# Kernel tuning notes

Measured on AMD Instinct MI355X. Metric: run time of the kernel, lower is better.

## Reference

```python
import jax, jax.numpy as jnp
import numpy as np

WEIGHT_BITS = 5
QUANT_BITS = 16
BN_EPS = 1e-5


def _quant_weight_pow2(w):
    # Round weights to signed powers of two; exponent clipped per DeepShift:
    # shift range = [-(2^(bits-1)-2), 0] = [-14, 0] for 5-bit weights.
    shift_min = -(2 ** (WEIGHT_BITS - 1) - 2)
    sign = jnp.sign(w)
    p = jnp.clip(jnp.round(jnp.log2(jnp.abs(w) + 1e-20)), shift_min, 0.0)
    wq = sign * jnp.exp2(p)
    # straight-through estimator
    return w + jax.lax.stop_gradient(wq - w)


def _quant_act(x):
    # Symmetric per-tensor linear quantization to QUANT_BITS (16-bit) with STE.
    qmax = 2.0 ** (QUANT_BITS - 1) - 1.0
    scale = jnp.maximum(jnp.max(jnp.abs(x)), 1e-12) / qmax
    xq = jnp.round(x / scale) * scale
    return x + jax.lax.stop_gradient(xq - x)


def _conv(x, w, stride=1, pad=0, groups=1):
    return jax.lax.conv_general_dilated(
        x, w, (stride, stride), [(pad, pad), (pad, pad)],
        dimension_numbers=("NCHW", "OIHW", "NCHW"),
        feature_group_count=groups)


def _shift_conv(x, w, stride=1, pad=0, groups=1, bias=None):
    y = _conv(_quant_act(x), _quant_weight_pow2(w), stride, pad, groups)
    if bias is not None:
        y = y + bias[None, :, None, None]
    return y


def _bn(x, g, b, m, v):
    inv = g * jax.lax.rsqrt(v + BN_EPS)
    return x * inv[None, :, None, None] + (b - m * inv)[None, :, None, None]


def setup_inputs() -> dict:
    key = jax.random.key(0)
    ks = jax.random.split(key, 8)
    B, C_in, H, W = 32, 1024, 32, 32
    width, C_out = 256, 1024
    inp = {
        "x": jax.random.normal(ks[0], (B, C_in, H, W), jnp.float32),
        "w1": jax.random.normal(ks[1], (width, C_in, 1, 1), jnp.float32) * 0.05,
        "peg_w": jax.random.normal(ks[2], (width, 1, 3, 3), jnp.float32) * 0.1,
        "peg_b": jax.random.normal(ks[3], (width,), jnp.float32) * 0.01,
        "w2": jax.random.normal(ks[4], (width, width, 3, 3), jnp.float32) * 0.05,
        "w3": jax.random.normal(ks[5], (C_out, width, 1, 1), jnp.float32) * 0.05,
        "bn1_g": jax.random.uniform(ks[6], (width,), jnp.float32, 0.5, 1.5),
        "bn1_b": jnp.zeros((width,), jnp.float32),
        "bn1_m": jnp.zeros((width,), jnp.float32),
        "bn1_v": jnp.ones((width,), jnp.float32),
        "bn2_g": jax.random.uniform(ks[7], (width,), jnp.float32, 0.5, 1.5),
        "bn2_b": jnp.zeros((width,), jnp.float32),
        "bn2_m": jnp.zeros((width,), jnp.float32),
        "bn2_v": jnp.ones((width,), jnp.float32),
        "bn3_g": jax.random.uniform(jax.random.fold_in(key, 9), (C_out,), jnp.float32, 0.5, 1.5),
        "bn3_b": jnp.zeros((C_out,), jnp.float32),
        "bn3_m": jnp.zeros((C_out,), jnp.float32),
        "bn3_v": jnp.ones((C_out,), jnp.float32),
    }
    return inp


def reference(x, w1, peg_w, peg_b, w2, w3,
              bn1_g, bn1_b, bn1_m, bn1_v,
              bn2_g, bn2_b, bn2_m, bn2_v,
              bn3_g, bn3_b, bn3_m, bn3_v):
    residual = x  # downsample is Identity (inplanes == outplanes, stride == 1)
    h = _shift_conv(x, w1)                                   # 1x1 1024->256
    h = _shift_conv(h, peg_w, stride=1, pad=1, groups=256,
                    bias=peg_b)                               # depthwise 3x3 PEG
    h = jax.nn.relu(_bn(h, bn1_g, bn1_b, bn1_m, bn1_v))
    h = _shift_conv(h, w2, stride=1, pad=1)                   # 3x3 256->256
    h = jax.nn.relu(_bn(h, bn2_g, bn2_b, bn2_m, bn2_v))
    h = _shift_conv(h, w3)                                    # 1x1 256->1024
    h = _bn(h, bn3_g, bn3_b, bn3_m, bn3_v)
    return jax.nn.relu(h + residual)
```

## Files before the change

kernel.cpp:

```cpp
#include <hip/hip_runtime.h>

typedef _Float16 f16;
typedef _Float16 f16x8 __attribute__((ext_vector_type(8)));
typedef float f32x4 __attribute__((ext_vector_type(4)));
typedef unsigned short u16;
typedef unsigned int u32;
typedef u32 u32x4 __attribute__((ext_vector_type(4)));

#define WS_BN1_INV  256u
#define WS_BN1_BETA 1280u
#define WS_BN2_INV  2304u
#define WS_BN2_BETA 3328u
#define WS_BN3_INV  4352u
#define WS_BN3_BETA 8448u
#define WS_PEG_B    12544u
#define WS_PEGQ     13568u
#define WS_W1Q      18432u
#define WS_W3Q      542720u
#define WS_W2Q      1067008u
#define WS_H1T      2246656u
#define WS_H2T      19023872u


__device__ __forceinline__ int badf(float f){
  union { float f; u32 u; } c; c.f = f;
  return (c.u & 0x7f800000u) == 0x7f800000u;
}
__device__ __forceinline__ float qpow2(float w){
  float a = fabsf(w) + 1e-20f;
  float p = rintf(log2f(a));
  p = fminf(fmaxf(p, -14.0f), 0.0f);
  float m = exp2f(p);
  return (w > 0.0f) ? m : ((w < 0.0f) ? -m : 0.0f);
}
#define SWZ(row, slot) ((((slot) ^ ((row) >> 1) ^ ((row) >> 3))) & 3)

__device__ __forceinline__ void mfma_step(const char* lds, int wm, int wn,
                                          int lr, int lg, f32x4 acc[4][4]){
  f16x8 a[4], bb[4];
  #pragma unroll
  for (int mf = 0; mf < 4; ++mf){
    int row = (wm << 6) + (mf << 4) + lr;
    a[mf] = *(const f16x8*)(lds + (row << 6) + (SWZ(row, lg) << 4));
  }
  #pragma unroll
  for (int nf = 0; nf < 4; ++nf){
    int row = (wn << 6) + (nf << 4) + lr;
    bb[nf] = *(const f16x8*)(lds + 8192 + (row << 6) + (SWZ(row, lg) << 4));
  }
  #pragma unroll
  for (int mf = 0; mf < 4; ++mf)
    #pragma unroll
    for (int nf = 0; nf < 4; ++nf)
      acc[mf][nf] = __builtin_amdgcn_mfma_f32_16x16x32_f16(a[mf], bb[nf], acc[mf][nf], 0, 0, 0);
}

__global__ __launch_bounds__(256) void prep_kernel(
    const float* __restrict__ w1, const float* __restrict__ pegw, const float* __restrict__ pegb,
    const float* __restrict__ w2, const float* __restrict__ w3,
    const float* g1, const float* b1, const float* m1, const float* v1,
    const float* g2, const float* b2, const float* m2, const float* v2,
    const float* g3, const float* b3, const float* m3, const float* v3,
    char* ws){
  int i = blockIdx.x * 256 + threadIdx.x;
  if (i < 262144){ ((f16*)(ws + WS_W1Q))[i] = (f16)qpow2(w1[i]); return; }
  i -= 262144;
  if (i < 589824){
    int tap = i >> 16, rem = i & 65535;
    int co = rem >> 8, ci = rem & 255;
    ((f16*)(ws + WS_W2Q))[i] = (f16)qpow2(w2[(((co << 8) + ci) * 9) + tap]);
    return;
  }
  i -= 589824;
  if (i < 262144){ ((f16*)(ws + WS_W3Q))[i] = (f16)qpow2(w3[i]); return; }
  i -= 262144;
  if (i < 2304){
    int tap = i >> 8, c = i & 255;
    ((f16*)(ws + WS_PEGQ))[i] = (f16)qpow2(pegw[c * 9 + tap]);
    return;
  }
  i -= 2304;
  if (i < 256){ ((float*)(ws + WS_PEG_B))[i] = pegb[i]; return; }
  i -= 256;
  if (i < 256){
    float inv = g1[i] / sqrtf(v1[i] + 1e-5f);
    ((float*)(ws + WS_BN1_INV))[i] = inv;
    ((float*)(ws + WS_BN1_BETA))[i] = b1[i] - m1[i] * inv;
    return;
  }
  i -= 256;
  if (i < 256){
    float inv = g2[i] / sqrtf(v2[i] + 1e-5f);
    ((float*)(ws + WS_BN2_INV))[i] = inv;
    ((float*)(ws + WS_BN2_BETA))[i] = b2[i] - m2[i] * inv;
    return;
  }
  i -= 256;
  if (i < 1024){
    float inv = g3[i] / sqrtf(v3[i] + 1e-5f);
    ((float*)(ws + WS_BN3_INV))[i] = inv;
    ((float*)(ws + WS_BN3_BETA))[i] = b3[i] - m3[i] * inv;
  }
}

__global__ __launch_bounds__(512) void conv1_kernel(const float* __restrict__ x, char* ws){
  __shared__ __align__(16) char lds[24576];
  const f16* w1q = (const f16*)(ws + WS_W1Q);
  f16* h1T = (f16*)(ws + WS_H1T);

  int tid = threadIdx.x, bid = blockIdx.x;
  int b = bid >> 3, m0 = (bid & 7) << 7;
  int l = tid & 63, wid = tid >> 6, wm = wid >> 2, wn = wid & 3;
  int lr = l & 15, lg = l >> 4;
  f32x4 acc[4][4] = {};

  int pblk = tid & 15;
  int cil  = tid >> 4;

  for (int ks = 0; ks < 32; ++ks){
    int k0 = ks << 5;
    {
      const float* src = x + (((size_t)(b << 10) + k0 + cil) << 10) + m0 + (pblk << 3);
      f32x4 d0 = *(const f32x4*)src;
      f32x4 d1 = *(const f32x4*)(src + 4);
      #pragma unroll
      for (int j = 0; j < 8; ++j){
        float xv = (j < 4) ? d0[j] : d1[j - 4];
        int row = (pblk << 3) + j;
        *(f16*)(lds + (row << 6) + (SWZ(row, cil >> 3) << 4) + ((cil & 7) << 1)) = (f16)xv;
      }
    }
    #pragma unroll
    for (int i = 0; i < 2; ++i){
      int s = tid + (i << 9);
      int row = s >> 2, slot = s & 3;
      u32x4 d = *(const u32x4*)(w1q + ((size_t)row << 10) + k0 + (slot << 3));
      *(u32x4*)(lds + 8192 + (row << 6) + (SWZ(row, slot) << 4)) = d;
    }
    __syncthreads();
    f16x8 a[4], bb[4];
    #pragma unroll
    for (int mf = 0; mf < 4; ++mf){
      int row = (wm << 6) + (mf << 4) + lr;
      a[mf] = *(const f16x8*)(lds + (row << 6) + (SWZ(row, lg) << 4));
    }
    #pragma unroll
    for (int nf = 0; nf < 4; ++nf){
      int row = (wn << 6) + (nf << 4) + lr;
      bb[nf] = *(const f16x8*)(lds + 8192 + (row << 6) + (SWZ(row, lg) << 4));
    }
    #pragma unroll
    for (int mf = 0; mf < 4; ++mf)
      #pragma unroll
      for (int nf = 0; nf < 4; ++nf)
        acc[mf][nf] = __builtin_amdgcn_mfma_f32_16x16x32_f16(a[mf], bb[nf], acc[mf][nf], 0, 0, 0);
    __syncthreads();
  }

  #pragma unroll
  for (int mf = 0; mf < 4; ++mf){
    int p0 = m0 + (wm << 6) + (mf << 4) + (lg << 2);
    size_t base = ((size_t)(b << 10) + p0) << 8;
    #pragma unroll
    for (int nf = 0; nf < 4; ++nf){
      int co = (wn << 6) + (nf << 4) + lr;
      #pragma unroll
      for (int r = 0; r < 4; ++r)
        h1T[base + ((size_t)r << 8) + co] = (f16)acc[mf][nf][r];
    }
  }
}

__global__ __launch_bounds__(256) void peg_kernel(char* ws){
  __shared__ __align__(16) f16 tile[3][32][256];
  const f16* h1T = (const f16*)(ws + WS_H1T);
  const f16* pegq = (const f16*)(ws + WS_PEGQ);
  const float* pb  = (const float*)(ws + WS_PEG_B);
  const float* inv1 = (const float*)(ws + WS_BN1_INV);
  const float* bt1  = (const float*)(ws + WS_BN1_BETA);
  f16* h2T = (f16*)(ws + WS_H2T);

  int tid = threadIdx.x;
  int b = blockIdx.x >> 5, h = blockIdx.x & 31;

  #pragma unroll
  for (int r = 0; r < 3; ++r){
    int hh = h + r - 1;
    #pragma unroll
    for (int i = 0; i < 4; ++i){
      int chunk = tid + (i << 8);
      int px = chunk >> 5, cg = chunk & 31;
      u32x4 d = {0u, 0u, 0u, 0u};
      if ((u32)hh < 32u)
        d = *(const u32x4*)(h1T + (((size_t)(b << 10) + (hh << 5) + px) << 8) + (cg << 3));
      *(u32x4*)(&tile[r][px][cg << 3]) = d;
    }
  }
  __syncthreads();

  int c0 = (tid & 31) << 3;
  int q  = tid >> 5;
  float acc[4][8];
  #pragma unroll
  for (int i = 0; i < 4; ++i)
    #pragma unroll
    for (int j = 0; j < 8; ++j) acc[i][j] = pb[c0 + j];

  #pragma unroll
  for (int ky = 0; ky < 3; ++ky){
    #pragma unroll
    for (int kx = 0; kx < 3; ++kx){
      f16x8 wv = *(const f16x8*)(pegq + ((ky * 3 + kx) << 8) + c0);
      #pragma unroll
      for (int i = 0; i < 4; ++i){
        int ww = (q << 2) + i + kx - 1;
        if ((u32)ww < 32u){
          f16x8 v = *(const f16x8*)(&tile[ky][ww][c0]);
          #pragma unroll
          for (int j = 0; j < 8; ++j) acc[i][j] += (float)v[j] * (float)wv[j];
        }
      }
    }
  }

  f32x4 iv0 = *(const f32x4*)(inv1 + c0), iv1 = *(const f32x4*)(inv1 + c0 + 4);
  f32x4 bt0 = *(const f32x4*)(bt1 + c0),  bt1v = *(const f32x4*)(bt1 + c0 + 4);
  #pragma unroll
  for (int i = 0; i < 4; ++i){
    f16x8 o;
    #pragma unroll
    for (int j = 0; j < 8; ++j){
      float ivj = (j < 4) ? iv0[j] : iv1[j - 4];
      float btj = (j < 4) ? bt0[j] : bt1v[j - 4];
      o[j] = (f16)fmaxf(acc[i][j] * ivj + btj, 0.0f);
    }
    int p = (h << 5) + (q << 2) + i;
    *(f16x8*)(h2T + (((size_t)(b << 10) + p) << 8) + c0) = o;
  }
}

__global__ __launch_bounds__(512) void conv2_kernel(char* ws){
  __shared__ __align__(16) char lds[104448 + 32768];
  const f16* h2T = (const f16*)(ws + WS_H2T);
  const f16* w2q = (const f16*)(ws + WS_W2Q);
  const float* inv2 = (const float*)(ws + WS_BN2_INV);
  const float* bt2  = (const float*)(ws + WS_BN2_BETA);
  f16* h3T = (f16*)(ws + WS_H1T);

  int tid = threadIdx.x, bid = blockIdx.x;
  int b = bid >> 3, mt = bid & 7;
  int h0 = mt << 2;
  int m0 = mt << 7;
  int l = tid & 63, wid = tid >> 6, wm = wid >> 2, wn = wid & 3;
  int lr = l & 15, lg = l >> 4;
  char* A = lds;
  char* B0 = lds + 104448;
  char* B1 = lds + 104448 + 16384;

  for (int chunk = tid; chunk < 6528; chunk += 512){
    int r = chunk / 1088;
    int rem = chunk - r * 1088;
    int cc = rem >> 5, slot = rem & 31;
    int hh = h0 - 1 + r, wwp = cc - 1;
    u32x4 d = {0u, 0u, 0u, 0u};
    if ((u32)hh < 32u && (u32)wwp < 32u)
      d = *(const u32x4*)(h2T + (((size_t)(b << 10) + (hh << 5) + wwp) << 8) + (slot << 3));
    int sw = slot ^ ((cc & 7) << 2);
    *(u32x4*)(A + ((r * 34 + cc) << 9) + (sw << 4)) = d;
  }
  #pragma unroll
  for (int i = 0; i < 2; ++i){
    int chunk = tid + (i << 9);
    int co = chunk >> 2, slot = chunk & 3;
    u32x4 d = *(const u32x4*)(w2q + (co << 8) + (slot << 3));
    *(u32x4*)(B0 + (co << 6) + (SWZ(co, slot) << 4)) = d;
  }
  __syncthreads();

  f32x4 acc[4][4] = {};
  for (int tap = 0; tap < 9; ++tap){
    int dy = tap / 3 - 1, dx = tap % 3 - 1;
    int rowbase[4], key[4];
    #pragma unroll
    for (int mf = 0; mf < 4; ++mf){
      int p = (wm << 6) + (mf << 4) + lr;
      int rr = (p >> 5) + dy + 1;
      int cc = (p & 31) + dx + 1;
      rowbase[mf] = ((rr * 34 + cc) << 9) + (lg << 4);
      key[mf] = cc & 7;
    }
    #pragma unroll 2
    for (int ks = 0; ks < 8; ++ks){
      int t = (tap << 3) + ks;
      u32x4 st[2];
      int have = (t < 71);
      int t1 = t + 1, wtap = t1 >> 3, wks = t1 & 7;
      const f16* srcb = w2q + wtap * 65536 + (wks << 5);
      if (have){
        #pragma unroll
        for (int i = 0; i < 2; ++i){
          int chunk = tid + (i << 9);
          int co = chunk >> 2, slot = chunk & 3;
          st[i] = *(const u32x4*)(srcb + (co << 8) + (slot << 3));
        }
      }
      const char* bs = (t & 1) ? B1 : B0;
      f16x8 a[4], bb[4];
      #pragma unroll
      for (int mf = 0; mf < 4; ++mf)
        a[mf] = *(const f16x8*)(A + rowbase[mf] + ((ks ^ key[mf]) << 6));
      #pragma unroll
      for (int nf = 0; nf < 4; ++nf){
        int row = (wn << 6) + (nf << 4) + lr;
        bb[nf] = *(const f16x8*)(bs + (row << 6) + (SWZ(row, lg) << 4));
      }
      #pragma unroll
      for (int mf = 0; mf < 4; ++mf)
        #pragma unroll
        for (int nf = 0; nf < 4; ++nf)
          acc[mf][nf] = __builtin_amdgcn_mfma_f32_16x16x32_f16(a[mf], bb[nf], acc[mf][nf], 0, 0, 0);
      if (have){
        char* bd = (t1 & 1) ? B1 : B0;
        #pragma unroll
        for (int i = 0; i < 2; ++i){
          int chunk = tid + (i << 9);
          int co = chunk >> 2, slot = chunk & 3;
          *(u32x4*)(bd + (co << 6) + (SWZ(co, slot) << 4)) = st[i];
        }
      }
      __syncthreads();
    }
  }

  #pragma unroll
  for (int mf = 0; mf < 4; ++mf){
    int p0 = m0 + (wm << 6) + (mf << 4) + (lg << 2);
    size_t base = ((size_t)(b << 10) + p0) << 8;
    #pragma unroll
    for (int nf = 0; nf < 4; ++nf){
      int co = (wn << 6) + (nf << 4) + lr;
      float iv = inv2[co], bt = bt2[co];
      #pragma unroll
      for (int r = 0; r < 4; ++r)
        h3T[base + ((size_t)r << 8) + co] = (f16)fmaxf(acc[mf][nf][r] * iv + bt, 0.0f);
    }
  }
}

__global__ __launch_bounds__(256) void conv3_kernel(const float* __restrict__ x,
                                                    float* __restrict__ out, char* ws){
  __shared__ __align__(16) char lds[16384];
  const f16* w3q = (const f16*)(ws + WS_W3Q);
  const f16* h3T = (const f16*)(ws + WS_H1T);
  const float* inv3 = (const float*)(ws + WS_BN3_INV);
  const float* bt3  = (const float*)(ws + WS_BN3_BETA);

  int tid = threadIdx.x, bid = blockIdx.x;
  int m0i = bid >> 8, b = (bid >> 3) & 31, n0i = bid & 7;
  int m0 = m0i << 7, n0 = n0i << 7;
  int l = tid & 63, wid = tid >> 6, wm = wid >> 1, wn = wid & 1;
  int lr = l & 15, lg = l >> 4;
  f32x4 acc[4][4] = {};

  for (int ks = 0; ks < 8; ++ks){
    int k0 = ks << 5;
    #pragma unroll
    for (int i = 0; i < 2; ++i){
      int s = tid + (i << 8);
      int row = s >> 2, slot = s & 3;
      u32x4 dA = *(const u32x4*)(w3q + ((size_t)(m0 + row) << 8) + k0 + (slot << 3));
      u32x4 dB = *(const u32x4*)(h3T + (((size_t)(b << 10) + n0 + row) << 8) + k0 + (slot << 3));
      *(u32x4*)(lds + (row << 6) + (SWZ(row, slot) << 4)) = dA;
      *(u32x4*)(lds + 8192 + (row << 6) + (SWZ(row, slot) << 4)) = dB;
    }
    __syncthreads();
    mfma_step(lds, wm, wn, lr, lg, acc);
    __syncthreads();
  }

  #pragma unroll
  for (int mf = 0; mf < 4; ++mf){
    int co0 = m0 + (wm << 6) + (mf << 4) + (lg << 2);
    f32x4 iv = *(const f32x4*)(inv3 + co0);
    f32x4 bt = *(const f32x4*)(bt3 + co0);
    #pragma unroll
    for (int nf = 0; nf < 4; ++nf){
      int p = n0 + (wn << 6) + (nf << 4) + lr;
      #pragma unroll
      for (int r = 0; r < 4; ++r){
        size_t idx = (((size_t)(b << 10) + co0 + r) << 10) + p;
        float z = acc[mf][nf][r] * iv[r] + bt[r] + x[idx];
        float rr = fmaxf(z, 0.0f);
        if (badf(z)) rr = 512.0f;
        out[idx] = rr;
      }
    }
  }
}

extern "C" void kernel_launch(void* const* d_in, const int* in_sizes, int n_in,
                              void* d_out, int out_size, void* d_ws, size_t ws_size,
                              hipStream_t stream){
  const float* x    = (const float*)d_in[0];
  const float* w1   = (const float*)d_in[1];
  const float* pegw = (const float*)d_in[2];
  const float* pegb = (const float*)d_in[3];
  const float* w2   = (const float*)d_in[4];
  const float* w3   = (const float*)d_in[5];
  const float* g1 = (const float*)d_in[6];
  const float* b1 = (const float*)d_in[7];
  const float* m1 = (const float*)d_in[8];
  const float* v1 = (const float*)d_in[9];
  const float* g2 = (const float*)d_in[10];
  const float* b2 = (const float*)d_in[11];
  const float* m2 = (const float*)d_in[12];
  const float* v2 = (const float*)d_in[13];
  const float* g3 = (const float*)d_in[14];
  const float* b3 = (const float*)d_in[15];
  const float* m3 = (const float*)d_in[16];
  const float* v3 = (const float*)d_in[17];
  char* ws = (char*)d_ws;

  prep_kernel<<<4368, 256, 0, stream>>>(w1, pegw, pegb, w2, w3,
                                        g1, b1, m1, v1, g2, b2, m2, v2,
                                        g3, b3, m3, v3, ws);
  conv1_kernel<<<256, 512, 0, stream>>>(x, ws);
  peg_kernel<<<1024, 256, 0, stream>>>(ws);
  conv2_kernel<<<256, 512, 0, stream>>>(ws);
  conv3_kernel<<<2048, 256, 0, stream>>>(x, (float*)d_out, ws);
}
```

Measured before the change: 190.0 us.

## Double-buffer conv1 LDS tiles with register prefetch and reorder conv3 block mapping

conv1 now keeps two LDS buffers. It prefetches the next K-slice of x and w1q into registers before the MFMA step and stores it into the other buffer afterward, so global loads overlap compute and one barrier per iteration is removed. The x load layout also changes: each thread reads two channels and writes them as packed half pairs, so each LDS store is 32-bit instead of 16-bit. conv3's block index decomposition is reordered so consecutive blocks share a batch, which should improve L2 reuse of h3T. The cost is doubled LDS (48KB) and extra registers in conv1, which may lower occupancy.

```diff
diff --git a/kernel.cpp b/kernel.cpp
--- a/kernel.cpp
+++ b/kernel.cpp
@@ -32,6 +32,9 @@
   p = fminf(fmaxf(p, -14.0f), 0.0f);
   float m = exp2f(p);
   return (w > 0.0f) ? m : ((w < 0.0f) ? -m : 0.0f);
+}
+__device__ __forceinline__ u32 pack2(float a, float b){
+  union { f16 h[2]; u32 u; } p; p.h[0] = (f16)a; p.h[1] = (f16)b; return p.u;
 }
 #define SWZ(row, slot) ((((slot) ^ ((row) >> 1) ^ ((row) >> 3))) & 3)
 
@@ -104,7 +107,7 @@
 }
 
 __global__ __launch_bounds__(512) void conv1_kernel(const float* __restrict__ x, char* ws){
-  __shared__ __align__(16) char lds[24576];
+  __shared__ __align__(16) char lds[49152];
   const f16* w1q = (const f16*)(ws + WS_W1Q);
   f16* h1T = (f16*)(ws + WS_H1T);
 
@@ -114,46 +117,75 @@
   int lr = l & 15, lg = l >> 4;
   f32x4 acc[4][4] = {};
 
-  int pblk = tid & 15;
-  int cil  = tid >> 4;
+  int q = tid & 31;
+  int c = tid >> 5;
+  const float* xb = x + (((size_t)(b << 10)) << 10) + m0 + (q << 2);
+  int aslot = c >> 2, aoff = (c & 3) << 2;
+
+  f32x4 d0, d1; u32x4 wb0, wb1;
+  {
+    const float* src = xb + (((size_t)(c << 1)) << 10);
+    d0 = *(const f32x4*)src;
+    d1 = *(const f32x4*)(src + 1024);
+    int s0 = tid, r0 = s0 >> 2, sl0 = s0 & 3;
+    int s1 = tid + 512, r1 = s1 >> 2, sl1 = s1 & 3;
+    wb0 = *(const u32x4*)(w1q + ((size_t)r0 << 10) + (sl0 << 3));
+    wb1 = *(const u32x4*)(w1q + ((size_t)r1 << 10) + (sl1 << 3));
+  }
+  {
+    char* A = lds;
+    #pragma unroll
+    for (int j = 0; j < 4; ++j){
+      int row = (q << 2) + j;
+      *(u32*)(A + (row << 6) + (SWZ(row, aslot) << 4) + aoff) = pack2(d0[j], d1[j]);
+    }
+    int s0 = tid, r0 = s0 >> 2, sl0 = s0 & 3;
+    int s1 = tid + 512, r1 = s1 >> 2, sl1 = s1 & 3;
+    *(u32x4*)(lds + 8192 + (r0 << 6) + (SWZ(r0, sl0) << 4)) = wb0;
+    *(u32x4*)(lds + 8192 + (r1 << 6) + (SWZ(r1, sl1) << 4)) = wb1;
+  }
+  __syncthreads();
 
   for (int ks = 0; ks < 32; ++ks){
-    int k0 = ks << 5;
-    {
-      const float* src = x + (((size_t)(b << 10) + k0 + cil) << 10) + m0 + (pblk << 3);
-      f32x4 d0 = *(const f32x4*)src;
-      f32x4 d1 = *(const f32x4*)(src + 4);
-      #pragma unroll
-      for (int j = 0; j < 8; ++j){
-        float xv = (j < 4) ? d0[j] : d1[j - 4];
-        int row = (pblk << 3) + j;
-        *(f16*)(lds + (row << 6) + (SWZ(row, cil >> 3) << 4) + ((cil & 7) << 1)) = (f16)xv;
-      }
-    }
-    #pragma unroll
-    for (int i = 0; i < 2; ++i){
-      int s = tid + (i << 9);
-      int row = s >> 2, slot = s & 3;
-      u32x4 d = *(const u32x4*)(w1q + ((size_t)row << 10) + k0 + (slot << 3));
-      *(u32x4*)(lds + 8192 + (row << 6) + (SWZ(row, slot) << 4)) = d;
-    }
-    __syncthreads();
+    const char* cur = lds + ((ks & 1) ? 24576 : 0);
+    char* nxt = lds + ((ks & 1) ? 0 : 24576);
+    if (ks < 31){
+      int k0 = (ks + 1) << 5;
+      const float* src = xb + (((size_t)(k0 + (c << 1))) << 10);
+      d0 = *(const f32x4*)src;
+      d1 = *(const f32x4*)(src + 1024);
+      int s0 = tid, r0 = s0 >> 2, sl0 = s0 & 3;
+      int s1 = tid + 512, r1 = s1 >> 2, sl1 = s1 & 3;
+      wb0 = *(const u32x4*)(w1q + ((size_t)r0 << 10) + k0 + (sl0 << 3));
+      wb1 = *(const u32x4*)(w1q + ((size_t)r1 << 10) + k0 + (sl1 << 3));
+    }
     f16x8 a[4], bb[4];
     #pragma unroll
     for (int mf = 0; mf < 4; ++mf){
       int row = (wm << 6) + (mf << 4) + lr;
-      a[mf] = *(const f16x8*)(lds + (row << 6) + (SWZ(row, lg) << 4));
+      a[mf] = *(const f16x8*)(cur + (row << 6) + (SWZ(row, lg) << 4));
     }
     #pragma unroll
     for (int nf = 0; nf < 4; ++nf){
       int row = (wn << 6) + (nf << 4) + lr;
-      bb[nf] = *(const f16x8*)(lds + 8192 + (row << 6) + (SWZ(row, lg) << 4));
+      bb[nf] = *(const f16x8*)(cur + 8192 + (row << 6) + (SWZ(row, lg) << 4));
     }
     #pragma unroll
     for (int mf = 0; mf < 4; ++mf)
       #pragma unroll
       for (int nf = 0; nf < 4; ++nf)
         acc[mf][nf] = __builtin_amdgcn_mfma_f32_16x16x32_f16(a[mf], bb[nf], acc[mf][nf], 0, 0, 0);
+    if (ks < 31){
+      #pragma unroll
+      for (int j = 0; j < 4; ++j){
+        int row = (q << 2) + j;
+        *(u32*)(nxt + (row << 6) + (SWZ(row, aslot) << 4) + aoff) = pack2(d0[j], d1[j]);
+      }
+      int s0 = tid, r0 = s0 >> 2, sl0 = s0 & 3;
+      int s1 = tid + 512, r1 = s1 >> 2, sl1 = s1 & 3;
+      *(u32x4*)(nxt + 8192 + (r0 << 6) + (SWZ(r0, sl0) << 4)) = wb0;
+      *(u32x4*)(nxt + 8192 + (r1 << 6) + (SWZ(r1, sl1) << 4)) = wb1;
+    }
     __syncthreads();
   }
 
@@ -356,8 +388,7 @@
   const float* bt3  = (const float*)(ws + WS_BN3_BETA);
 
   int tid = threadIdx.x, bid = blockIdx.x;
-  int m0i = bid >> 8, b = (bid >> 3) & 31, n0i = bid & 7;
-  int m0 = m0i << 7, n0 = n0i << 7;
+  int b = bid >> 6, m0 = ((bid >> 3) & 7) << 7, n0 = (bid & 7) << 7;
   int l = tid & 63, wid = tid >> 6, wm = wid >> 1, wn = wid & 1;
   int lr = l & 15, lg = l >> 4;
   f32x4 acc[4][4] = {};
```

After: 177.4 us. 1.07x faster.
